# Kernel tuning notes

Measured on AMD Instinct MI355X. Metric: run time of the kernel, lower is better.

The kernel has to match this reference:

```python
import jax, jax.numpy as jnp
import numpy as np

K = 1024       # num_embeddings
D = 64         # embedding_dim
DECAY = 0.99
COMMIT = 0.25
EPS = 1e-05


def setup_inputs() -> dict:
    key = jax.random.key(0)
    k1, k2, k3 = jax.random.split(key, 3)
    x = jax.random.normal(k1, (16, 64, 64, 64), jnp.float32)  # NCHW, C == D
    embedding_weight = jax.random.normal(k2, (K, D), jnp.float32)
    ema_weight = jax.random.normal(k3, (K, D), jnp.float32)
    ema_cluster_size = jnp.zeros((K,), jnp.float32)
    return {"x": x, "embedding_weight": embedding_weight,
            "ema_cluster_size": ema_cluster_size, "ema_weight": ema_weight}


def reference(x, embedding_weight, ema_cluster_size, ema_weight):
    # NCHW -> NHWC, flatten tokens
    xp = jnp.transpose(x, (0, 2, 3, 1))            # [B,H,W,D]
    flat = xp.reshape(-1, D)                        # [N,D]
    dists = ((flat ** 2).sum(1, keepdims=True)
             + (embedding_weight ** 2).sum(1)
             - 2.0 * flat @ embedding_weight.T)     # [N,K]
    idx = jnp.argmin(dists, axis=1)                 # [N]
    encodings = jax.nn.one_hot(idx, K, dtype=flat.dtype)  # [N,K]
    quantized = jnp.take(embedding_weight, idx, axis=0).reshape(xp.shape)
    # training-mode EMA updates (scatter-add instead of dense one-hot matmuls)
    counts = jnp.zeros((K,), flat.dtype).at[idx].add(1.0)
    new_cs = ema_cluster_size * DECAY + (1.0 - DECAY) * counts
    n = new_cs.sum()
    new_cs = (new_cs + EPS) / (n + K * EPS) * n     # Laplace smoothing
    dw = jnp.zeros((K, D), flat.dtype).at[idx].add(flat)
    new_ema_weight = ema_weight * DECAY + (1.0 - DECAY) * dw
    new_embedding = new_ema_weight / new_cs[:, None]
    # commitment loss and straight-through estimator
    e_latent_loss = jnp.mean((jax.lax.stop_gradient(quantized) - xp) ** 2)
    loss = COMMIT * e_latent_loss
    q_st = xp + jax.lax.stop_gradient(quantized - xp)
    return (loss, jnp.transpose(q_st, (0, 3, 1, 2)), encodings,
            new_embedding, new_cs, new_ema_weight)
```

## Files before the change

### kernel.cpp

```cpp
#include <hip/hip_runtime.h>

#define DECAYF 0.99f
#define ONEMF 0.01f
#define EPSF 1e-5f

typedef __bf16 bf16x8 __attribute__((ext_vector_type(8)));
typedef float f32x4 __attribute__((ext_vector_type(4)));
typedef unsigned short ushort8 __attribute__((ext_vector_type(8)));

#define WS_COUNTS 65536
#define WS_NCHALF 66560
#define WS_SSE    67584
#define WS_EHI    67600
#define WS_ELO    100368

__device__ __forceinline__ float wave_reduce_add(float v) {
#pragma unroll
    for (int o = 32; o > 0; o >>= 1) v += __shfl_xor(v, o, 64);
    return v;
}

__device__ __forceinline__ unsigned short bf_rne(float f) {
    unsigned int u = __float_as_uint(f);
    unsigned int r = u + 0x7fffu + ((u >> 16) & 1u);
    return (unsigned short)(r >> 16);
}

__global__ __launch_bounds__(256) void prep_kernel(const float* __restrict__ E,
                                                   float* __restrict__ ws) {
    const int bid = blockIdx.x, tid = threadIdx.x;
    const int id = bid * 256 + tid;
    ws[id] = 0.0f;
    if (bid < 4) ws[WS_COUNTS + bid * 256 + tid] = 0.0f;
    if (bid == 4 && tid == 0) ws[WS_SSE] = 0.0f;
    const float v = E[id];
    const unsigned short h = bf_rne(v);
    const float hf = __uint_as_float((unsigned int)h << 16);
    const unsigned short l = bf_rne(v - hf);
    ((unsigned short*)(ws + WS_EHI))[id] = h;
    ((unsigned short*)(ws + WS_ELO))[id] = l;
    const int lane = tid & 63;
    const float s = wave_reduce_add(v * v);
    if (lane == 0) ws[WS_NCHALF + (id >> 6)] = -0.5f * s;
}

__global__ __launch_bounds__(256, 2) void vq_main(const float* __restrict__ x,
                                                  const float* __restrict__ E,
                                                  float* __restrict__ out,
                                                  float* __restrict__ ws) {
    const int tid = threadIdx.x;
    const int lane = tid & 63;
    const int w = tid >> 6;
    const int blk = blockIdx.x;
    const int b = blk >> 5;
    const int hw0 = (blk & 31) << 7;
    const int tok0 = blk << 7;

    __shared__ float xs[128 * 68];
    __shared__ int i1sh[128], i2sh[128], idx_sh[128];

    float* enc = out + 1 + (size_t)4194304;
    f32x4* encb4 = (f32x4*)(enc + (size_t)tok0 * 1024);

    {
        const float* xb = x + ((size_t)b << 18) + hw0;
#pragma unroll
        for (int cc = 0; cc < 32; ++cc) {
            const int id = cc * 256 + tid;
            const int c = id >> 7, t = id & 127;
            xs[t * 68 + c] = xb[((size_t)c << 12) + t];
        }
    }
    __syncthreads();

    const int q = lane >> 4, m = lane & 15;

    bf16x8 Ah[2][2], Al[2][2];
#pragma unroll
    for (int t = 0; t < 2; ++t) {
        const int tok = w * 32 + t * 16 + m;
#pragma unroll
        for (int s = 0; s < 2; ++s) {
            const float* p = &xs[tok * 68 + s * 32 + q * 8];
            ushort8 hu, lu;
#pragma unroll
            for (int j = 0; j < 8; ++j) {
                const float f = p[j];
                const unsigned short h = bf_rne(f);
                const float hf = __uint_as_float((unsigned int)h << 16);
                hu[j] = h;
                lu[j] = bf_rne(f - hf);
            }
            Ah[t][s] = __builtin_bit_cast(bf16x8, hu);
            Al[t][s] = __builtin_bit_cast(bf16x8, lu);
        }
    }

    const ushort8* __restrict__ Ehp = (const ushort8*)(ws + WS_EHI);
    const ushort8* __restrict__ Elp = (const ushort8*)(ws + WS_ELO);
    const float* __restrict__ ncp = ws + WS_NCHALF;

    float b1[2][4], b2[2][4];
    int i1[2][4], i2[2][4];
#pragma unroll
    for (int t = 0; t < 2; ++t)
#pragma unroll
        for (int r = 0; r < 4; ++r) { b1[t][r] = -1e30f; b2[t][r] = -1e30f; i1[t][r] = 0; i2[t][r] = 1; }

    ushort8 p0h[2], p1h[2], p0l[2], p1l[2];
    float pnc[2];
#pragma unroll
    for (int s = 0; s < 2; ++s) {
        const int code = s * 16 + m;
        p0h[s] = Ehp[code * 8 + q];
        p1h[s] = Ehp[code * 8 + 4 + q];
        p0l[s] = Elp[code * 8 + q];
        p1l[s] = Elp[code * 8 + 4 + q];
        pnc[s] = ncp[code];
    }

    const f32x4 z4 = {0.0f, 0.0f, 0.0f, 0.0f};

#define VQ_STEP(S, CK)                                                          \
    {                                                                           \
        const bf16x8 bh0 = __builtin_bit_cast(bf16x8, p0h[S]);                  \
        const bf16x8 bh1 = __builtin_bit_cast(bf16x8, p1h[S]);                  \
        const bf16x8 bl0 = __builtin_bit_cast(bf16x8, p0l[S]);                  \
        const bf16x8 bl1 = __builtin_bit_cast(bf16x8, p1l[S]);                  \
        const float nc = pnc[S];                                                \
        if ((CK) + 2 < 64) {                                                    \
            const int code = ((CK) + 2) * 16 + m;                               \
            p0h[S] = Ehp[code * 8 + q];                                         \
            p1h[S] = Ehp[code * 8 + 4 + q];                                     \
            p0l[S] = Elp[code * 8 + q];                                         \
            p1l[S] = Elp[code * 8 + 4 + q];                                     \
            pnc[S] = ncp[code];                                                 \
        }                                                                       \
           \
        {                                                                       \
            const int zslot = (CK) * 512 + tid;                                 \
            __builtin_nontemporal_store(z4, encb4 + zslot);                     \
            __builtin_nontemporal_store(z4, encb4 + zslot + 256);               \
        }                                                                       \
        const int idx = (CK) * 16 + m;                                          \
        _Pragma("unroll")                                                       \
        for (int t = 0; t < 2; ++t) {                                           \
            f32x4 acc = {nc, nc, nc, nc};         \
            acc = __builtin_amdgcn_mfma_f32_16x16x32_bf16(Ah[t][0], bh0, acc, 0, 0, 0); \
            acc = __builtin_amdgcn_mfma_f32_16x16x32_bf16(Ah[t][1], bh1, acc, 0, 0, 0); \
            acc = __builtin_amdgcn_mfma_f32_16x16x32_bf16(Al[t][0], bh0, acc, 0, 0, 0); \
            acc = __builtin_amdgcn_mfma_f32_16x16x32_bf16(Al[t][1], bh1, acc, 0, 0, 0); \
            acc = __builtin_amdgcn_mfma_f32_16x16x32_bf16(Ah[t][0], bl0, acc, 0, 0, 0); \
            acc = __builtin_amdgcn_mfma_f32_16x16x32_bf16(Ah[t][1], bl1, acc, 0, 0, 0); \
            _Pragma("unroll")                                                   \
            for (int r = 0; r < 4; ++r) {                                       \
                const float s = acc[r];                                         \
                const bool cA = s > b1[t][r];                                   \
                const bool cB = s > b2[t][r];                                   \
                b2[t][r] = cA ? b1[t][r] : (cB ? s : b2[t][r]);                 \
                i2[t][r] = cA ? i1[t][r] : (cB ? idx : i2[t][r]);               \
                b1[t][r] = cA ? s : b1[t][r];                                   \
                i1[t][r] = cA ? idx : i1[t][r];                                 \
            }                                                                   \
        }                                                                       \
    }

    for (int j = 0; j < 32; ++j) {
        VQ_STEP(0, 2 * j)
        VQ_STEP(1, 2 * j + 1)
    }
#undef VQ_STEP

#pragma unroll
    for (int d = 1; d < 16; d <<= 1) {
#pragma unroll
        for (int t = 0; t < 2; ++t)
#pragma unroll
            for (int r = 0; r < 4; ++r) {
                const float ob1 = __shfl_xor(b1[t][r], d, 64);
                const int   oi1 = __shfl_xor(i1[t][r], d, 64);
                const float ob2 = __shfl_xor(b2[t][r], d, 64);
                const int   oi2 = __shfl_xor(i2[t][r], d, 64);
                const bool wv = ob1 > b1[t][r];
                const float t1 = wv ? ob1 : b1[t][r]; const int ti1 = wv ? oi1 : i1[t][r];
                const float sA = wv ? b1[t][r] : ob1; const int siA = wv ? i1[t][r] : oi1;
                const float sB = wv ? ob2 : b2[t][r]; const int siB = wv ? oi2 : i2[t][r];
                const bool w2 = sB > sA;
                b1[t][r] = t1; i1[t][r] = ti1;
                b2[t][r] = w2 ? sB : sA; i2[t][r] = w2 ? siB : siA;
            }
    }
    if (m == 0) {
#pragma unroll
        for (int t = 0; t < 2; ++t)
#pragma unroll
            for (int r = 0; r < 4; ++r) {
                const int tokL = w * 32 + t * 16 + q * 4 + r;
                i1sh[tokL] = i1[t][r];
                i2sh[tokL] = i2[t][r];
            }
    }

    float dval = 0.0f;
    if (lane < 32) {
        const int tokL = w * 32 + lane;
        const int I1 = i1sh[tokL], I2 = i2sh[tokL];
        const int ca = I1 < I2 ? I1 : I2;
        const int cb = I1 < I2 ? I2 : I1;
        const float* Ea = E + ca * 64;
        const float* Eb = E + cb * 64;
        const float* xr = &xs[tokL * 68];
        double sa = 0, ea = 0, sb = 0, eb = 0, x2 = 0;
#pragma unroll 8
        for (int c = 0; c < 64; ++c) {
            const double xv = (double)xr[c];
            const double va = (double)Ea[c], vb = (double)Eb[c];
            sa += xv * va; ea += va * va;
            sb += xv * vb; eb += vb * vb;
            x2 += xv * xv;
        }
        const double qa = ea - 2.0 * sa;
        const double qb = eb - 2.0 * sb;
        int best; double qq;
        if (qb < qa) { best = cb; qq = qb; } else { best = ca; qq = qa; }
        idx_sh[tokL] = best;
        float dd = (float)(qq + x2);
        dval = dd < 0.f ? 0.f : dd;
        atomicAdd(&ws[WS_COUNTS + best], 1.0f);
    }
    const float ssum = wave_reduce_add(dval);
    if (lane == 0) atomicAdd(&ws[WS_SSE], ssum);
    __syncthreads();

    float* outq = out + 1;
#pragma unroll
    for (int cc = 0; cc < 32; ++cc) {
        const int id = cc * 256 + tid;
        const int c = id >> 7, t = id & 127;
        const int kb = idx_sh[t];
        const float xv = xs[t * 68 + c];
        const float eq = E[kb * 64 + c];
        outq[((size_t)(b * 64 + c) << 12) + hw0 + t] = xv + (eq - xv);
    }
#pragma unroll 4
    for (int tt = 0; tt < 32; ++tt) {
        const int t = w * 32 + tt;
        const int kb = idx_sh[t];
        atomicAdd(&ws[kb * 64 + lane], xs[t * 68 + lane]);
    }
    {
        if (tid < 128) {
            const int kb = idx_sh[tid];
            __builtin_nontemporal_store(1.0f, enc + (size_t)(tok0 + tid) * 1024 + kb);
        }
    }
}

__global__ __launch_bounds__(1024) void fin_cs(const float* __restrict__ cs_in,
                                               float* __restrict__ out,
                                               const float* __restrict__ ws) {
    __shared__ float red[16];
    __shared__ float n_sh;
    const int tid = threadIdx.x;
    const float raw = cs_in[tid] * DECAYF + ONEMF * ws[WS_COUNTS + tid];
    const float s = wave_reduce_add(raw);
    if ((tid & 63) == 0) red[tid >> 6] = s;
    __syncthreads();
    if (tid == 0) {
        float n = 0.f;
#pragma unroll
        for (int i = 0; i < 16; ++i) n += red[i];
        n_sh = n;
        out[0] = 0.25f * ws[WS_SSE] * (1.0f / 4194304.0f);
    }
    __syncthreads();
    const float n = n_sh;
    out[71368705 + tid] = (raw + EPSF) / (n + 1024.0f * EPSF) * n;
}

__global__ __launch_bounds__(256) void fin_w(const float* __restrict__ emaw,
                                             float* __restrict__ out,
                                             const float* __restrict__ ws) {
    const int i = blockIdx.x * 256 + threadIdx.x;
    const float val = emaw[i] * DECAYF + ONEMF * ws[i];
    out[71369729 + i] = val;
    const float cs = out[71368705 + (i >> 6)];
    out[71303169 + i] = val / cs;
}

extern "C" void kernel_launch(void* const* d_in, const int* in_sizes, int n_in,
                              void* d_out, int out_size, void* d_ws, size_t ws_size,
                              hipStream_t stream) {
    const float* x    = (const float*)d_in[0];
    const float* E    = (const float*)d_in[1];
    const float* cs   = (const float*)d_in[2];
    const float* emaw = (const float*)d_in[3];
    float* out = (float*)d_out;
    float* ws  = (float*)d_ws;

    prep_kernel<<<256, 256, 0, stream>>>(E, ws);
    vq_main<<<512, 256, 0, stream>>>(x, E, out, ws);
    fin_cs<<<1, 1024, 0, stream>>>(cs, out, ws);
    fin_w<<<256, 256, 0, stream>>>(emaw, out, ws);
}
```

Baseline: 381.4 us.

## Stage codebook chunks through double-buffered swizzled LDS instead of per-wave global loads

Codebook hi/lo bf16 rows and norms were previously loaded straight from global memory by every wave with register prefetch. They are now loaded cooperatively, 32 codes per chunk, into a double-buffered XOR-swizzled LDS region. Each wave then reads its MFMA B operands from LDS. This is meant to cut redundant global/L2 traffic across the four waves, at the cost of a __syncthreads per chunk and about 16KB of extra LDS, which may affect occupancy.

```diff
diff --git a/kernel.cpp b/kernel.cpp
--- a/kernel.cpp
+++ b/kernel.cpp
@@ -51,6 +51,7 @@
     const int tid = threadIdx.x;
     const int lane = tid & 63;
     const int w = tid >> 6;
+    const int q = lane >> 4, m = lane & 15;
     const int blk = blockIdx.x;
     const int b = blk >> 5;
     const int hw0 = (blk & 31) << 7;
@@ -58,9 +59,14 @@
 
     __shared__ float xs[128 * 68];
     __shared__ int i1sh[128], i2sh[128], idx_sh[128];
+    __shared__ char lds_b[2][8320];
 
     float* enc = out + 1 + (size_t)4194304;
     f32x4* encb4 = (f32x4*)(enc + (size_t)tok0 * 1024);
+
+    const unsigned short* __restrict__ EHIu = (const unsigned short*)(ws + WS_EHI);
+    const unsigned short* __restrict__ ELOu = (const unsigned short*)(ws + WS_ELO);
+    const float* __restrict__ ncp = ws + WS_NCHALF;
 
     {
         const float* xb = x + ((size_t)b << 18) + hw0;
@@ -71,9 +77,14 @@
             xs[t * 68 + c] = xb[((size_t)c << 12) + t];
         }
     }
+
+    const int cl_s = tid >> 3, g_s = tid & 7;
+    const int dst_s = cl_s * 128 + ((g_s ^ (cl_s & 7)) << 4);
+
+    *(f32x4*)(lds_b[0] + dst_s)        = *(const f32x4*)(EHIu + tid * 8);
+    *(f32x4*)(lds_b[0] + 4096 + dst_s) = *(const f32x4*)(ELOu + tid * 8);
+    if (tid < 32) *(float*)(lds_b[0] + 8192 + tid * 4) = ncp[tid];
     __syncthreads();
-
-    const int q = lane >> 4, m = lane & 15;
 
     bf16x8 Ah[2][2], Al[2][2];
 #pragma unroll
@@ -96,10 +107,6 @@
         }
     }
 
-    const ushort8* __restrict__ Ehp = (const ushort8*)(ws + WS_EHI);
-    const ushort8* __restrict__ Elp = (const ushort8*)(ws + WS_ELO);
-    const float* __restrict__ ncp = ws + WS_NCHALF;
-
     float b1[2][4], b2[2][4];
     int i1[2][4], i2[2][4];
 #pragma unroll
@@ -107,42 +114,35 @@
 #pragma unroll
         for (int r = 0; r < 4; ++r) { b1[t][r] = -1e30f; b2[t][r] = -1e30f; i1[t][r] = 0; i2[t][r] = 1; }
 
-    ushort8 p0h[2], p1h[2], p0l[2], p1l[2];
-    float pnc[2];
-#pragma unroll
-    for (int s = 0; s < 2; ++s) {
-        const int code = s * 16 + m;
-        p0h[s] = Ehp[code * 8 + q];
-        p1h[s] = Ehp[code * 8 + 4 + q];
-        p0l[s] = Elp[code * 8 + q];
-        p1l[s] = Elp[code * 8 + 4 + q];
-        pnc[s] = ncp[code];
-    }
-
     const f32x4 z4 = {0.0f, 0.0f, 0.0f, 0.0f};
-
-#define VQ_STEP(S, CK)                                                          \
+    const int hm = m & 7;
+    const int off0 = (q ^ hm) << 4;
+    const int off1 = ((4 + q) ^ hm) << 4;
+
+    for (int kc = 0; kc < 32; ++kc) {
+        f32x4 sH = z4, sL = z4; float sN = 0.0f;
+        if (kc < 31) {
+            sH = *(const f32x4*)(EHIu + (kc + 1) * 2048 + tid * 8);
+            sL = *(const f32x4*)(ELOu + (kc + 1) * 2048 + tid * 8);
+            if (tid < 32) sN = ncp[(kc + 1) * 32 + tid];
+        }
+        const char* bufc = lds_b[kc & 1];
+
+#define VQ_STEP(S)                                                              \
     {                                                                           \
-        const bf16x8 bh0 = __builtin_bit_cast(bf16x8, p0h[S]);                  \
-        const bf16x8 bh1 = __builtin_bit_cast(bf16x8, p1h[S]);                  \
-        const bf16x8 bl0 = __builtin_bit_cast(bf16x8, p0l[S]);                  \
-        const bf16x8 bl1 = __builtin_bit_cast(bf16x8, p1l[S]);                  \
-        const float nc = pnc[S];                                                \
-        if ((CK) + 2 < 64) {                                                    \
-            const int code = ((CK) + 2) * 16 + m;                               \
-            p0h[S] = Ehp[code * 8 + q];                                         \
-            p1h[S] = Ehp[code * 8 + 4 + q];                                     \
-            p0l[S] = Elp[code * 8 + q];                                         \
-            p1l[S] = Elp[code * 8 + 4 + q];                                     \
-            pnc[S] = ncp[code];                                                 \
-        }                                                                       \
-           \
-        {                                                                       \
-            const int zslot = (CK) * 512 + tid;                                 \
+        const int cl = (S) * 16 + m;                                            \
+        const char* rowp = bufc + cl * 128;                                     \
+        const bf16x8 bh0 = *(const bf16x8*)(rowp + off0);                       \
+        const bf16x8 bh1 = *(const bf16x8*)(rowp + off1);                       \
+        const bf16x8 bl0 = *(const bf16x8*)(rowp + 4096 + off0);                \
+        const bf16x8 bl1 = *(const bf16x8*)(rowp + 4096 + off1);                \
+        const float nc = *(const float*)(bufc + 8192 + cl * 4);                 \
+        {        \
+            const int zslot = (kc * 2 + (S)) * 512 + tid;                       \
             __builtin_nontemporal_store(z4, encb4 + zslot);                     \
             __builtin_nontemporal_store(z4, encb4 + zslot + 256);               \
         }                                                                       \
-        const int idx = (CK) * 16 + m;                                          \
+        const int idx = kc * 32 + cl;                                           \
         _Pragma("unroll")                                                       \
         for (int t = 0; t < 2; ++t) {                                           \
             f32x4 acc = {nc, nc, nc, nc};         \
@@ -165,11 +165,18 @@
         }                                                                       \
     }
 
-    for (int j = 0; j < 32; ++j) {
-        VQ_STEP(0, 2 * j)
-        VQ_STEP(1, 2 * j + 1)
-    }
+        VQ_STEP(0)
+        VQ_STEP(1)
 #undef VQ_STEP
+
+        if (kc < 31) {
+            char* bufn = lds_b[(kc + 1) & 1];
+            *(f32x4*)(bufn + dst_s)        = sH;
+            *(f32x4*)(bufn + 4096 + dst_s) = sL;
+            if (tid < 32) *(float*)(bufn + 8192 + tid * 4) = sN;
+        }
+        __syncthreads();
+    }
 
 #pragma unroll
     for (int d = 1; d < 16; d <<= 1) {
```

After: 363.5 us. 4.7% less time.
